# Kernel optimization log

Measured on AMD Instinct MI355X. Metric: run time of the kernel, lower is better.

Reference implementation:

```python
import jax, jax.numpy as jnp
import numpy as np

N_RAW, N1, N2, K, D, OUT = 200000, 100000, 20000, 10, 256, 256

def setup_inputs() -> dict:
    key = jax.random.key(0)
    ks = jax.random.split(key, 8)
    scale1 = (6.0 / (OUT + 2 * D)) ** 0.5   # xavier_uniform bound
    scale2 = (6.0 / (OUT + 2 * OUT)) ** 0.5
    return {
        "raw_features": jax.random.normal(ks[0], (N_RAW, D), dtype=jnp.float32),
        "W1": jax.random.uniform(ks[1], (OUT, 2 * D), jnp.float32, -scale1, scale1),
        "W2": jax.random.uniform(ks[2], (OUT, 2 * OUT), jnp.float32, -scale2, scale2),
        "nodes1": jax.random.randint(ks[3], (N1,), 0, N_RAW),
        "neigh1": jax.random.randint(ks[4], (N1, K), 0, N_RAW),
        "self2": jax.random.randint(ks[5], (N2,), 0, N1),
        "neigh2": jax.random.randint(ks[6], (N2, K), 0, N1),
    }

def _sage_layer(embs, self_idx, neigh_idx, W):
    # segment-mean over sampled neighbors (MEAN agg with fixed fanout K)
    agg = jnp.mean(embs[neigh_idx], axis=1)          # [n, d]
    combined = jnp.concatenate([embs[self_idx], agg], axis=1)  # [n, 2d]
    # F.relu(W.mm(combined.t())).t() == relu(combined @ W.T)
    return jax.nn.relu(combined @ W.T)

def reference(raw_features, W1, W2, nodes1, neigh1, self2, neigh2):
    h1 = _sage_layer(raw_features, nodes1, neigh1, W1)  # [N1, OUT]
    h2 = _sage_layer(h1, self2, neigh2, W2)             # [N2, OUT]
    return h2
```

## Files before the change

### kernel.cpp

```cpp
#include <hip/hip_runtime.h>
#include <hip/hip_bf16.h>


typedef __attribute__((ext_vector_type(8))) short bf16x8;
typedef __attribute__((ext_vector_type(4))) float f32x4;

static __device__ __forceinline__ short f2bf(float f) {
  __hip_bfloat16 h = __float2bfloat16(f);
  return *reinterpret_cast<short*>(&h);
}
static __device__ __forceinline__ float bf2f(short s) {
  union { unsigned u; float f; } x;
  x.u = ((unsigned)(unsigned short)s) << 16;
  return x.f;
}

__global__ __launch_bounds__(256) void convert_all(
    const float* __restrict__ raw, const float* __restrict__ W1,
    const float* __restrict__ W2, short* __restrict__ rawb,
    short* __restrict__ W1b, short* __restrict__ W2b) {
  const int b = blockIdx.x;
  const float* src;
  short* dst;
  size_t base;
  if (b < 25000) { src = raw; dst = rawb; base = (size_t)b * 2048; }
  else if (b < 25064) { src = W1; dst = W1b; base = (size_t)(b - 25000) * 2048; }
  else { src = W2; dst = W2b; base = (size_t)(b - 25064) * 2048; }
  const size_t i = base + (size_t)threadIdx.x * 8;
  const float4* s4 = reinterpret_cast<const float4*>(src + i);
  float4 u = s4[0], v = s4[1];
  bf16x8 o;
  o[0] = f2bf(u.x); o[1] = f2bf(u.y); o[2] = f2bf(u.z); o[3] = f2bf(u.w);
  o[4] = f2bf(v.x); o[5] = f2bf(v.y); o[6] = f2bf(v.z); o[7] = f2bf(v.w);
  *reinterpret_cast<bf16x8*>(dst + i) = o;
}

template <bool OUT_BF16>
__global__ __launch_bounds__(256, 4) void sage_fused(
    const short* __restrict__ E,
    const int* __restrict__ self_idx,
    const int* __restrict__ neigh,
    const short* __restrict__ Wb,
    void* __restrict__ out) {
  __shared__ short As[32][520];

  const int tid = threadIdx.x;
  const int m0 = blockIdx.x * 32;

  {
    const int c = tid & 31;
    const int rs = tid >> 5;
#pragma unroll
    for (int rr = 0; rr < 4; ++rr) {
      const int r = rs * 4 + rr;
      const int gr = m0 + r;
      const int si = self_idx[gr];
      int nb[10];
#pragma unroll
      for (int k = 0; k < 10; ++k) nb[k] = neigh[gr * 10 + k];
      bf16x8 sv = *reinterpret_cast<const bf16x8*>(E + (size_t)si * 256 + c * 8);
      bf16x8 v[10];
#pragma unroll
      for (int k = 0; k < 10; ++k)
        v[k] = *reinterpret_cast<const bf16x8*>(E + (size_t)nb[k] * 256 + c * 8);
      bf16x8 mv;
#pragma unroll
      for (int j = 0; j < 8; ++j) {
        float sA = bf2f(v[0][j]) + bf2f(v[2][j]) + bf2f(v[4][j]) + bf2f(v[6][j]) + bf2f(v[8][j]);
        float sB = bf2f(v[1][j]) + bf2f(v[3][j]) + bf2f(v[5][j]) + bf2f(v[7][j]) + bf2f(v[9][j]);
        mv[j] = f2bf((sA + sB) * 0.1f);
      }
      *reinterpret_cast<bf16x8*>(&As[r][c * 8]) = sv;
      *reinterpret_cast<bf16x8*>(&As[r][256 + c * 8]) = mv;
    }
  }
  __syncthreads();

  const int wave = tid >> 6, lane = tid & 63;
  const int wn = wave * 64;
  const int lr = lane & 15;
  const int lkb = (lane >> 4) * 8;
  const short* Bp = Wb + (size_t)(wn + lr) * 512 + lkb;

  f32x4 acc[2][4] = {};

  bf16x8 a0 = *reinterpret_cast<const bf16x8*>(&As[lr][lkb]);
  bf16x8 a1 = *reinterpret_cast<const bf16x8*>(&As[16 + lr][lkb]);
  bf16x8 b0 = *reinterpret_cast<const bf16x8*>(Bp + 0 * 8192);
  bf16x8 b1 = *reinterpret_cast<const bf16x8*>(Bp + 1 * 8192);
  bf16x8 b2 = *reinterpret_cast<const bf16x8*>(Bp + 2 * 8192);
  bf16x8 b3 = *reinterpret_cast<const bf16x8*>(Bp + 3 * 8192);

#pragma unroll
  for (int ks = 0; ks < 16; ++ks) {
    bf16x8 na0, na1, nb0, nb1, nb2, nb3;
    if (ks < 15) {
      const int k0 = (ks + 1) * 32;
      na0 = *reinterpret_cast<const bf16x8*>(&As[lr][k0 + lkb]);
      na1 = *reinterpret_cast<const bf16x8*>(&As[16 + lr][k0 + lkb]);
      nb0 = *reinterpret_cast<const bf16x8*>(Bp + k0 + 0 * 8192);
      nb1 = *reinterpret_cast<const bf16x8*>(Bp + k0 + 1 * 8192);
      nb2 = *reinterpret_cast<const bf16x8*>(Bp + k0 + 2 * 8192);
      nb3 = *reinterpret_cast<const bf16x8*>(Bp + k0 + 3 * 8192);
    }
    __builtin_amdgcn_s_setprio(1);
    acc[0][0] = __builtin_amdgcn_mfma_f32_16x16x32_bf16(a0, b0, acc[0][0], 0, 0, 0);
    acc[1][0] = __builtin_amdgcn_mfma_f32_16x16x32_bf16(a1, b0, acc[1][0], 0, 0, 0);
    acc[0][1] = __builtin_amdgcn_mfma_f32_16x16x32_bf16(a0, b1, acc[0][1], 0, 0, 0);
    acc[1][1] = __builtin_amdgcn_mfma_f32_16x16x32_bf16(a1, b1, acc[1][1], 0, 0, 0);
    acc[0][2] = __builtin_amdgcn_mfma_f32_16x16x32_bf16(a0, b2, acc[0][2], 0, 0, 0);
    acc[1][2] = __builtin_amdgcn_mfma_f32_16x16x32_bf16(a1, b2, acc[1][2], 0, 0, 0);
    acc[0][3] = __builtin_amdgcn_mfma_f32_16x16x32_bf16(a0, b3, acc[0][3], 0, 0, 0);
    acc[1][3] = __builtin_amdgcn_mfma_f32_16x16x32_bf16(a1, b3, acc[1][3], 0, 0, 0);
    __builtin_amdgcn_s_setprio(0);
    a0 = na0; a1 = na1; b0 = nb0; b1 = nb1; b2 = nb2; b3 = nb3;
  }

#pragma unroll
  for (int mi = 0; mi < 2; ++mi)
#pragma unroll
    for (int ni = 0; ni < 4; ++ni)
#pragma unroll
      for (int r = 0; r < 4; ++r) {
        const int gm = m0 + mi * 16 + (lane >> 4) * 4 + r;
        const int gn = wn + ni * 16 + lr;
        float v = acc[mi][ni][r];
        v = v > 0.f ? v : 0.f;
        if (OUT_BF16)
          reinterpret_cast<short*>(out)[(size_t)gm * 256 + gn] = f2bf(v);
        else
          reinterpret_cast<float*>(out)[(size_t)gm * 256 + gn] = v;
      }
}

extern "C" void kernel_launch(void* const* d_in, const int* in_sizes, int n_in,
                              void* d_out, int out_size, void* d_ws, size_t ws_size,
                              hipStream_t stream) {
  const float* raw = (const float*)d_in[0];
  const float* W1 = (const float*)d_in[1];
  const float* W2 = (const float*)d_in[2];
  const int* nodes1 = (const int*)d_in[3];
  const int* neigh1 = (const int*)d_in[4];
  const int* self2 = (const int*)d_in[5];
  const int* neigh2 = (const int*)d_in[6];
  float* out = (float*)d_out;

  const int N_RAW = 200000, N1 = 100000, N2 = 20000;

  short* rawb = (short*)d_ws;
  short* h1 = rawb + (size_t)N_RAW * 256;
  short* W1b = h1 + (size_t)N1 * 256;
  short* W2b = W1b + 131072;

  convert_all<<<25128, 256, 0, stream>>>(raw, W1, W2, rawb, W1b, W2b);
  sage_fused<true><<<N1 / 32, 256, 0, stream>>>(rawb, nodes1, neigh1, W1b, h1);
  sage_fused<false><<<N2 / 32, 256, 0, stream>>>(h1, self2, neigh2, W2b, out);
}
```

Before: 226.0 us.

## Warp-specialize sage kernel into persistent producer/consumer with double-buffered LDS

Replaces the one-tile-per-block kernels with persistent 512-thread blocks in which four waves gather and mean-aggregate the next 32-row tile into a second LDS buffer while the other four waves run the MFMA GEMM on the current tile. The aim is to hide the random-gather latency behind matrix compute. The raw-feature conversion also switches to nontemporal loads. The cost is twice the LDS per block, a fixed grid of 512 blocks, and a block-wide barrier per tile that couples the two halves.

```diff
diff --git a/kernel.cpp b/kernel.cpp
--- a/kernel.cpp
+++ b/kernel.cpp
@@ -27,8 +27,9 @@
   else if (b < 25064) { src = W1; dst = W1b; base = (size_t)(b - 25000) * 2048; }
   else { src = W2; dst = W2b; base = (size_t)(b - 25064) * 2048; }
   const size_t i = base + (size_t)threadIdx.x * 8;
-  const float4* s4 = reinterpret_cast<const float4*>(src + i);
-  float4 u = s4[0], v = s4[1];
+  const f32x4* s4 = reinterpret_cast<const f32x4*>(src + i);
+  f32x4 u = __builtin_nontemporal_load(s4);
+  f32x4 v = __builtin_nontemporal_load(s4 + 1);
   bf16x8 o;
   o[0] = f2bf(u.x); o[1] = f2bf(u.y); o[2] = f2bf(u.z); o[3] = f2bf(u.w);
   o[4] = f2bf(v.x); o[5] = f2bf(v.y); o[6] = f2bf(v.z); o[7] = f2bf(v.w);
@@ -36,33 +37,35 @@
 }
 
 template <bool OUT_BF16>
-__global__ __launch_bounds__(256, 4) void sage_fused(
+__global__ __launch_bounds__(512, 4) void sage_pc(
     const short* __restrict__ E,
     const int* __restrict__ self_idx,
     const int* __restrict__ neigh,
     const short* __restrict__ Wb,
-    void* __restrict__ out) {
-  __shared__ short As[32][520];
+    void* __restrict__ out,
+    int ntiles) {
+  __shared__ short As[2][32][520];
 
   const int tid = threadIdx.x;
-  const int m0 = blockIdx.x * 32;
+  const int nblk = gridDim.x;
+  const int t0 = blockIdx.x;
 
-  {
+  auto gather = [&](int t, int buf) __attribute__((always_inline)) {
     const int c = tid & 31;
     const int rs = tid >> 5;
 #pragma unroll
     for (int rr = 0; rr < 4; ++rr) {
       const int r = rs * 4 + rr;
-      const int gr = m0 + r;
+      const int gr = t * 32 + r;
       const int si = self_idx[gr];
-      int nb[10];
+      int nbx[10];
 #pragma unroll
-      for (int k = 0; k < 10; ++k) nb[k] = neigh[gr * 10 + k];
+      for (int k = 0; k < 10; ++k) nbx[k] = neigh[gr * 10 + k];
       bf16x8 sv = *reinterpret_cast<const bf16x8*>(E + (size_t)si * 256 + c * 8);
       bf16x8 v[10];
 #pragma unroll
       for (int k = 0; k < 10; ++k)
-        v[k] = *reinterpret_cast<const bf16x8*>(E + (size_t)nb[k] * 256 + c * 8);
+        v[k] = *reinterpret_cast<const bf16x8*>(E + (size_t)nbx[k] * 256 + c * 8);
       bf16x8 mv;
 #pragma unroll
       for (int j = 0; j < 8; ++j) {
@@ -70,67 +73,79 @@
         float sB = bf2f(v[1][j]) + bf2f(v[3][j]) + bf2f(v[5][j]) + bf2f(v[7][j]) + bf2f(v[9][j]);
         mv[j] = f2bf((sA + sB) * 0.1f);
       }
-      *reinterpret_cast<bf16x8*>(&As[r][c * 8]) = sv;
-      *reinterpret_cast<bf16x8*>(&As[r][256 + c * 8]) = mv;
+      *reinterpret_cast<bf16x8*>(&As[buf][r][c * 8]) = sv;
+      *reinterpret_cast<bf16x8*>(&As[buf][r][256 + c * 8]) = mv;
     }
-  }
+  };
+
+  if (tid < 256) gather(t0, 0);
   __syncthreads();
 
-  const int wave = tid >> 6, lane = tid & 63;
-  const int wn = wave * 64;
-  const int lr = lane & 15;
-  const int lkb = (lane >> 4) * 8;
-  const short* Bp = Wb + (size_t)(wn + lr) * 512 + lkb;
+  int buf = 0;
+  for (int t = t0; t < ntiles; t += nblk, buf ^= 1) {
+    if (tid < 256) {
+      const int tn = t + nblk;
+      if (tn < ntiles) gather(tn, buf ^ 1);
+    } else {
+      const int wave = (tid >> 6) - 4;
+      const int lane = tid & 63;
+      const int wn = wave * 64;
+      const int lr = lane & 15;
+      const int lkb = (lane >> 4) * 8;
+      const short* Bp = Wb + (size_t)(wn + lr) * 512 + lkb;
 
-  f32x4 acc[2][4] = {};
+      f32x4 acc[2][4] = {};
 
-  bf16x8 a0 = *reinterpret_cast<const bf16x8*>(&As[lr][lkb]);
-  bf16x8 a1 = *reinterpret_cast<const bf16x8*>(&As[16 + lr][lkb]);
-  bf16x8 b0 = *reinterpret_cast<const bf16x8*>(Bp + 0 * 8192);
-  bf16x8 b1 = *reinterpret_cast<const bf16x8*>(Bp + 1 * 8192);
-  bf16x8 b2 = *reinterpret_cast<const bf16x8*>(Bp + 2 * 8192);
-  bf16x8 b3 = *reinterpret_cast<const bf16x8*>(Bp + 3 * 8192);
+      bf16x8 a0 = *reinterpret_cast<const bf16x8*>(&As[buf][lr][lkb]);
+      bf16x8 a1 = *reinterpret_cast<const bf16x8*>(&As[buf][16 + lr][lkb]);
+      bf16x8 b0 = *reinterpret_cast<const bf16x8*>(Bp + 0 * 8192);
+      bf16x8 b1 = *reinterpret_cast<const bf16x8*>(Bp + 1 * 8192);
+      bf16x8 b2 = *reinterpret_cast<const bf16x8*>(Bp + 2 * 8192);
+      bf16x8 b3 = *reinterpret_cast<const bf16x8*>(Bp + 3 * 8192);
 
 #pragma unroll
-  for (int ks = 0; ks < 16; ++ks) {
-    bf16x8 na0, na1, nb0, nb1, nb2, nb3;
-    if (ks < 15) {
-      const int k0 = (ks + 1) * 32;
-      na0 = *reinterpret_cast<const bf16x8*>(&As[lr][k0 + lkb]);
-      na1 = *reinterpret_cast<const bf16x8*>(&As[16 + lr][k0 + lkb]);
-      nb0 = *reinterpret_cast<const bf16x8*>(Bp + k0 + 0 * 8192);
-      nb1 = *reinterpret_cast<const bf16x8*>(Bp + k0 + 1 * 8192);
-      nb2 = *reinterpret_cast<const bf16x8*>(Bp + k0 + 2 * 8192);
-      nb3 = *reinterpret_cast<const bf16x8*>(Bp + k0 + 3 * 8192);
-    }
-    __builtin_amdgcn_s_setprio(1);
-    acc[0][0] = __builtin_amdgcn_mfma_f32_16x16x32_bf16(a0, b0, acc[0][0], 0, 0, 0);
-    acc[1][0] = __builtin_amdgcn_mfma_f32_16x16x32_bf16(a1, b0, acc[1][0], 0, 0, 0);
-    acc[0][1] = __builtin_amdgcn_mfma_f32_16x16x32_bf16(a0, b1, acc[0][1], 0, 0, 0);
-    acc[1][1] = __builtin_amdgcn_mfma_f32_16x16x32_bf16(a1, b1, acc[1][1], 0, 0, 0);
-    acc[0][2] = __builtin_amdgcn_mfma_f32_16x16x32_bf16(a0, b2, acc[0][2], 0, 0, 0);
-    acc[1][2] = __builtin_amdgcn_mfma_f32_16x16x32_bf16(a1, b2, acc[1][2], 0, 0, 0);
-    acc[0][3] = __builtin_amdgcn_mfma_f32_16x16x32_bf16(a0, b3, acc[0][3], 0, 0, 0);
-    acc[1][3] = __builtin_amdgcn_mfma_f32_16x16x32_bf16(a1, b3, acc[1][3], 0, 0, 0);
-    __builtin_amdgcn_s_setprio(0);
-    a0 = na0; a1 = na1; b0 = nb0; b1 = nb1; b2 = nb2; b3 = nb3;
-  }
+      for (int ks = 0; ks < 16; ++ks) {
+        bf16x8 na0, na1, nb0, nb1, nb2, nb3;
+        if (ks < 15) {
+          const int k0 = (ks + 1) * 32;
+          na0 = *reinterpret_cast<const bf16x8*>(&As[buf][lr][k0 + lkb]);
+          na1 = *reinterpret_cast<const bf16x8*>(&As[buf][16 + lr][k0 + lkb]);
+          nb0 = *reinterpret_cast<const bf16x8*>(Bp + k0 + 0 * 8192);
+          nb1 = *reinterpret_cast<const bf16x8*>(Bp + k0 + 1 * 8192);
+          nb2 = *reinterpret_cast<const bf16x8*>(Bp + k0 + 2 * 8192);
+          nb3 = *reinterpret_cast<const bf16x8*>(Bp + k0 + 3 * 8192);
+        }
+        __builtin_amdgcn_s_setprio(1);
+        acc[0][0] = __builtin_amdgcn_mfma_f32_16x16x32_bf16(a0, b0, acc[0][0], 0, 0, 0);
+        acc[1][0] = __builtin_amdgcn_mfma_f32_16x16x32_bf16(a1, b0, acc[1][0], 0, 0, 0);
+        acc[0][1] = __builtin_amdgcn_mfma_f32_16x16x32_bf16(a0, b1, acc[0][1], 0, 0, 0);
+        acc[1][1] = __builtin_amdgcn_mfma_f32_16x16x32_bf16(a1, b1, acc[1][1], 0, 0, 0);
+        acc[0][2] = __builtin_amdgcn_mfma_f32_16x16x32_bf16(a0, b2, acc[0][2], 0, 0, 0);
+        acc[1][2] = __builtin_amdgcn_mfma_f32_16x16x32_bf16(a1, b2, acc[1][2], 0, 0, 0);
+        acc[0][3] = __builtin_amdgcn_mfma_f32_16x16x32_bf16(a0, b3, acc[0][3], 0, 0, 0);
+        acc[1][3] = __builtin_amdgcn_mfma_f32_16x16x32_bf16(a1, b3, acc[1][3], 0, 0, 0);
+        __builtin_amdgcn_s_setprio(0);
+        a0 = na0; a1 = na1; b0 = nb0; b1 = nb1; b2 = nb2; b3 = nb3;
+      }
 
 #pragma unroll
-  for (int mi = 0; mi < 2; ++mi)
+      for (int mi = 0; mi < 2; ++mi)
 #pragma unroll
-    for (int ni = 0; ni < 4; ++ni)
+        for (int ni = 0; ni < 4; ++ni)
 #pragma unroll
-      for (int r = 0; r < 4; ++r) {
-        const int gm = m0 + mi * 16 + (lane >> 4) * 4 + r;
-        const int gn = wn + ni * 16 + lr;
-        float v = acc[mi][ni][r];
-        v = v > 0.f ? v : 0.f;
-        if (OUT_BF16)
-          reinterpret_cast<short*>(out)[(size_t)gm * 256 + gn] = f2bf(v);
-        else
-          reinterpret_cast<float*>(out)[(size_t)gm * 256 + gn] = v;
-      }
+          for (int r = 0; r < 4; ++r) {
+            const int gm = t * 32 + mi * 16 + (lane >> 4) * 4 + r;
+            const int gn = wn + ni * 16 + lr;
+            float v = acc[mi][ni][r];
+            v = v > 0.f ? v : 0.f;
+            if (OUT_BF16)
+              reinterpret_cast<short*>(out)[(size_t)gm * 256 + gn] = f2bf(v);
+            else
+              reinterpret_cast<float*>(out)[(size_t)gm * 256 + gn] = v;
+          }
+    }
+    __syncthreads();
+  }
 }
 
 extern "C" void kernel_launch(void* const* d_in, const int* in_sizes, int n_in,
@@ -145,7 +160,7 @@
   const int* neigh2 = (const int*)d_in[6];
   float* out = (float*)d_out;
 
-  const int N_RAW = 200000, N1 = 100000, N2 = 20000;
+  const int N_RAW = 200000, N1 = 100000;
 
   short* rawb = (short*)d_ws;
   short* h1 = rawb + (size_t)N_RAW * 256;
@@ -153,6 +168,6 @@
   short* W2b = W1b + 131072;
 
   convert_all<<<25128, 256, 0, stream>>>(raw, W1, W2, rawb, W1b, W2b);
-  sage_fused<true><<<N1 / 32, 256, 0, stream>>>(rawb, nodes1, neigh1, W1b, h1);
-  sage_fused<false><<<N2 / 32, 256, 0, stream>>>(h1, self2, neigh2, W2b, out);
+  sage_pc<true><<<512, 512, 0, stream>>>(rawb, nodes1, neigh1, W1b, h1, 3125);
+  sage_pc<false><<<512, 512, 0, stream>>>(h1, self2, neigh2, W2b, out, 625);
 }
```

New measurement: 285.0 us. +26.1%, slower.

## Double threads per block to split gather and GEMM across eight waves

Applied to the files above, without the earlier changes.

The fused SAGE kernel now uses 512 threads per block. Each thread gathers two rows instead of four, and each wave computes a 32-column slice instead of 64, so accumulator and register pressure drop and more waves are available to hide gather latency. The explicit register double-buffering of the A/B fragments is removed in favour of plain loads each k-step. The fp32-to-bf16 conversion switches to nontemporal loads to avoid polluting cache. The risk is less latency hiding inside the MFMA loop and launch bounds (512,8) that may not be achievable given the LDS size.

```diff
diff --git a/kernel.cpp b/kernel.cpp
--- a/kernel.cpp
+++ b/kernel.cpp
@@ -27,8 +27,9 @@
   else if (b < 25064) { src = W1; dst = W1b; base = (size_t)(b - 25000) * 2048; }
   else { src = W2; dst = W2b; base = (size_t)(b - 25064) * 2048; }
   const size_t i = base + (size_t)threadIdx.x * 8;
-  const float4* s4 = reinterpret_cast<const float4*>(src + i);
-  float4 u = s4[0], v = s4[1];
+  const f32x4* s4 = reinterpret_cast<const f32x4*>(src + i);
+  f32x4 u = __builtin_nontemporal_load(s4);
+  f32x4 v = __builtin_nontemporal_load(s4 + 1);
   bf16x8 o;
   o[0] = f2bf(u.x); o[1] = f2bf(u.y); o[2] = f2bf(u.z); o[3] = f2bf(u.w);
   o[4] = f2bf(v.x); o[5] = f2bf(v.y); o[6] = f2bf(v.z); o[7] = f2bf(v.w);
@@ -36,7 +37,7 @@
 }
 
 template <bool OUT_BF16>
-__global__ __launch_bounds__(256, 4) void sage_fused(
+__global__ __launch_bounds__(512, 8) void sage_fused(
     const short* __restrict__ E,
     const int* __restrict__ self_idx,
     const int* __restrict__ neigh,
@@ -46,80 +47,61 @@
 
   const int tid = threadIdx.x;
   const int m0 = blockIdx.x * 32;
+  const int c = tid & 31;
+  const int rs = tid >> 5;
 
-  {
-    const int c = tid & 31;
-    const int rs = tid >> 5;
 #pragma unroll
-    for (int rr = 0; rr < 4; ++rr) {
-      const int r = rs * 4 + rr;
-      const int gr = m0 + r;
-      const int si = self_idx[gr];
-      int nb[10];
+  for (int rr = 0; rr < 2; ++rr) {
+    const int r = rs * 2 + rr;
+    const int gr = m0 + r;
+    const int si = self_idx[gr];
+    int nbx[10];
 #pragma unroll
-      for (int k = 0; k < 10; ++k) nb[k] = neigh[gr * 10 + k];
-      bf16x8 sv = *reinterpret_cast<const bf16x8*>(E + (size_t)si * 256 + c * 8);
-      bf16x8 v[10];
+    for (int k = 0; k < 10; ++k) nbx[k] = neigh[gr * 10 + k];
+    bf16x8 sv = *reinterpret_cast<const bf16x8*>(E + (size_t)si * 256 + c * 8);
+    bf16x8 v[10];
 #pragma unroll
-      for (int k = 0; k < 10; ++k)
-        v[k] = *reinterpret_cast<const bf16x8*>(E + (size_t)nb[k] * 256 + c * 8);
-      bf16x8 mv;
+    for (int k = 0; k < 10; ++k)
+      v[k] = *reinterpret_cast<const bf16x8*>(E + (size_t)nbx[k] * 256 + c * 8);
+    bf16x8 mv;
 #pragma unroll
-      for (int j = 0; j < 8; ++j) {
-        float sA = bf2f(v[0][j]) + bf2f(v[2][j]) + bf2f(v[4][j]) + bf2f(v[6][j]) + bf2f(v[8][j]);
-        float sB = bf2f(v[1][j]) + bf2f(v[3][j]) + bf2f(v[5][j]) + bf2f(v[7][j]) + bf2f(v[9][j]);
-        mv[j] = f2bf((sA + sB) * 0.1f);
-      }
-      *reinterpret_cast<bf16x8*>(&As[r][c * 8]) = sv;
-      *reinterpret_cast<bf16x8*>(&As[r][256 + c * 8]) = mv;
+    for (int j = 0; j < 8; ++j) {
+      float sA = bf2f(v[0][j]) + bf2f(v[2][j]) + bf2f(v[4][j]) + bf2f(v[6][j]) + bf2f(v[8][j]);
+      float sB = bf2f(v[1][j]) + bf2f(v[3][j]) + bf2f(v[5][j]) + bf2f(v[7][j]) + bf2f(v[9][j]);
+      mv[j] = f2bf((sA + sB) * 0.1f);
     }
+    *reinterpret_cast<bf16x8*>(&As[r][c * 8]) = sv;
+    *reinterpret_cast<bf16x8*>(&As[r][256 + c * 8]) = mv;
   }
   __syncthreads();
 
   const int wave = tid >> 6, lane = tid & 63;
-  const int wn = wave * 64;
+  const int wn = wave * 32;
   const int lr = lane & 15;
   const int lkb = (lane >> 4) * 8;
   const short* Bp = Wb + (size_t)(wn + lr) * 512 + lkb;
 
-  f32x4 acc[2][4] = {};
-
-  bf16x8 a0 = *reinterpret_cast<const bf16x8*>(&As[lr][lkb]);
-  bf16x8 a1 = *reinterpret_cast<const bf16x8*>(&As[16 + lr][lkb]);
-  bf16x8 b0 = *reinterpret_cast<const bf16x8*>(Bp + 0 * 8192);
-  bf16x8 b1 = *reinterpret_cast<const bf16x8*>(Bp + 1 * 8192);
-  bf16x8 b2 = *reinterpret_cast<const bf16x8*>(Bp + 2 * 8192);
-  bf16x8 b3 = *reinterpret_cast<const bf16x8*>(Bp + 3 * 8192);
+  f32x4 acc[2][2] = {};
 
 #pragma unroll
   for (int ks = 0; ks < 16; ++ks) {
-    bf16x8 na0, na1, nb0, nb1, nb2, nb3;
-    if (ks < 15) {
-      const int k0 = (ks + 1) * 32;
-      na0 = *reinterpret_cast<const bf16x8*>(&As[lr][k0 + lkb]);
-      na1 = *reinterpret_cast<const bf16x8*>(&As[16 + lr][k0 + lkb]);
-      nb0 = *reinterpret_cast<const bf16x8*>(Bp + k0 + 0 * 8192);
-      nb1 = *reinterpret_cast<const bf16x8*>(Bp + k0 + 1 * 8192);
-      nb2 = *reinterpret_cast<const bf16x8*>(Bp + k0 + 2 * 8192);
-      nb3 = *reinterpret_cast<const bf16x8*>(Bp + k0 + 3 * 8192);
-    }
+    const int k0 = ks * 32;
+    bf16x8 a0 = *reinterpret_cast<const bf16x8*>(&As[lr][k0 + lkb]);
+    bf16x8 a1 = *reinterpret_cast<const bf16x8*>(&As[16 + lr][k0 + lkb]);
+    bf16x8 b0 = *reinterpret_cast<const bf16x8*>(Bp + k0);
+    bf16x8 b1 = *reinterpret_cast<const bf16x8*>(Bp + k0 + 8192);
     __builtin_amdgcn_s_setprio(1);
     acc[0][0] = __builtin_amdgcn_mfma_f32_16x16x32_bf16(a0, b0, acc[0][0], 0, 0, 0);
     acc[1][0] = __builtin_amdgcn_mfma_f32_16x16x32_bf16(a1, b0, acc[1][0], 0, 0, 0);
     acc[0][1] = __builtin_amdgcn_mfma_f32_16x16x32_bf16(a0, b1, acc[0][1], 0, 0, 0);
     acc[1][1] = __builtin_amdgcn_mfma_f32_16x16x32_bf16(a1, b1, acc[1][1], 0, 0, 0);
-    acc[0][2] = __builtin_amdgcn_mfma_f32_16x16x32_bf16(a0, b2, acc[0][2], 0, 0, 0);
-    acc[1][2] = __builtin_amdgcn_mfma_f32_16x16x32_bf16(a1, b2, acc[1][2], 0, 0, 0);
-    acc[0][3] = __builtin_amdgcn_mfma_f32_16x16x32_bf16(a0, b3, acc[0][3], 0, 0, 0);
-    acc[1][3] = __builtin_amdgcn_mfma_f32_16x16x32_bf16(a1, b3, acc[1][3], 0, 0, 0);
     __builtin_amdgcn_s_setprio(0);
-    a0 = na0; a1 = na1; b0 = nb0; b1 = nb1; b2 = nb2; b3 = nb3;
   }
 
 #pragma unroll
   for (int mi = 0; mi < 2; ++mi)
 #pragma unroll
-    for (int ni = 0; ni < 4; ++ni)
+    for (int ni = 0; ni < 2; ++ni)
 #pragma unroll
       for (int r = 0; r < 4; ++r) {
         const int gm = m0 + mi * 16 + (lane >> 4) * 4 + r;
@@ -145,7 +127,7 @@
   const int* neigh2 = (const int*)d_in[6];
   float* out = (float*)d_out;
 
-  const int N_RAW = 200000, N1 = 100000, N2 = 20000;
+  const int N_RAW = 200000, N1 = 100000;
 
   short* rawb = (short*)d_ws;
   short* h1 = rawb + (size_t)N_RAW * 256;
@@ -153,6 +135,6 @@
   short* W2b = W1b + 131072;
 
   convert_all<<<25128, 256, 0, stream>>>(raw, W1, W2, rawb, W1b, W2b);
-  sage_fused<true><<<N1 / 32, 256, 0, stream>>>(rawb, nodes1, neigh1, W1b, h1);
-  sage_fused<false><<<N2 / 32, 256, 0, stream>>>(h1, self2, neigh2, W2b, out);
+  sage_fused<true><<<3125, 512, 0, stream>>>(rawb, nodes1, neigh1, W1b, h1);
+  sage_fused<false><<<625, 512, 0, stream>>>(h1, self2, neigh2, W2b, out);
 }
```

New measurement: 226.4 us. No clear change (+0.2%).
